# Kernel tuning notes

Hardware: AMD Instinct MI355X
Metric: run time of the kernel (lower is better)

The kernel has to match this reference:

```python
import jax, jax.numpy as jnp
import numpy as np

N_NODES = 100000
N_EDGES = 1250000
IN_DIM = 128
HID_DIM = 64
OUT_DIM = 16


def setup_inputs() -> dict:
    key = jax.random.key(0)
    k1, k2, k3, k4, k5, k6, k7 = jax.random.split(key, 7)
    x = jax.random.normal(k1, (N_NODES, IN_DIM), dtype=jnp.float32)
    edge_index = jax.random.randint(k2, (2, N_EDGES), 0, N_NODES, dtype=jnp.int64)
    s = 1.0 / np.sqrt(IN_DIM)
    W1 = jax.random.uniform(k3, (IN_DIM, HID_DIM), jnp.float32, -s, s)
    b1 = jax.random.uniform(k4, (HID_DIM,), jnp.float32, -s, s)
    s2 = 1.0 / np.sqrt(HID_DIM)
    W2 = jax.random.uniform(k5, (HID_DIM, OUT_DIM), jnp.float32, -s2, s2)
    b2 = jax.random.uniform(k6, (OUT_DIM,), jnp.float32, -s2, s2)
    return {"x": x, "edge_index": edge_index, "W1": W1, "b1": b1, "W2": W2, "b2": b2}


def reference(x, edge_index, W1, b1, W2, b2):
    # GCNConv (PyG default): linear transform, add self-loops, symmetric norm,
    # gather-scatter aggregation, bias. Then relu -> linear -> log_softmax.
    N = x.shape[0]
    loop = jnp.arange(N, dtype=edge_index.dtype)
    src = jnp.concatenate([edge_index[0], loop])  # message sources
    dst = jnpp_concat = jnp.concatenate([edge_index[1], loop])  # message targets
    # degree (with self-loops) computed on destination nodes
    deg = jax.ops.segment_sum(jnp.ones_like(dst, dtype=x.dtype), dst, num_segments=N)
    deg_inv_sqrt = jnp.where(deg > 0, jax.lax.rsqrt(deg), 0.0)
    norm = deg_inv_sqrt[src] * deg_inv_sqrt[dst]  # [E+N]
    h = x @ W1  # [N, hid] -- transform before aggregation (fewer bytes moved)
    msg = h[src] * norm[:, None]  # gather: [E+N, hid]
    agg = jax.ops.segment_sum(msg, dst, num_segments=N) + b1  # scatter-add
    h = jax.nn.relu(agg)
    logits = h @ W2 + b2
    return jax.nn.log_softmax(logits, axis=-1)
```

## Files before the change

kernel.cpp:

```cpp
#include <hip/hip_runtime.h>
#include <hip/hip_bf16.h>

#define N_NODES 100000
#define N_EDGES 1250000
#define IN_DIM  128
#define HID     64
#define OUTD    16
#define ROW     64
#define NRANGE  8
#define RSIZE   12500
#define NCHUNK  128
#define CHUNK   9768
#define FILLB   (NRANGE * NCHUNK)
#define MTILE   128
#define GEMMB   ((N_NODES + MTILE - 1) / MTILE)

typedef __attribute__((ext_vector_type(8))) short  short8;
typedef __attribute__((ext_vector_type(4))) float  floatx4;

__device__ __forceinline__ unsigned short f2bf(float f) {
    unsigned u = __float_as_uint(f);
    u += 0x7fffu + ((u >> 16) & 1u);
    return (unsigned short)(u >> 16);
}
__device__ __forceinline__ unsigned pk2(float lo, float hi) {
    __hip_bfloat162 t = __float22bfloat162_rn(make_float2(lo, hi));
    return *reinterpret_cast<unsigned*>(&t);
}
__device__ __forceinline__ float bf2f_lo(unsigned u) { return __uint_as_float(u << 16); }
__device__ __forceinline__ float bf2f_hi(unsigned u) { return __uint_as_float(u & 0xffff0000u); }

__global__ __launch_bounds__(256) void zero_cursor(int* __restrict__ cursor,
                                                   unsigned* __restrict__ hb_dummy) {
    int i = blockIdx.x * 256 + threadIdx.x;
    if (i < N_NODES) cursor[i] = 0;
    if (i < 32) hb_dummy[i] = 0u;
}

__global__ __launch_bounds__(256) void fill_gemm(const float* __restrict__ x,
                                                 const float* __restrict__ W1,
                                                 const int* __restrict__ src,
                                                 const int* __restrict__ dst,
                                                 int* __restrict__ cursor,
                                                 int* __restrict__ csr,
                                                 unsigned short* __restrict__ hb) {
    __shared__ unsigned short w1t[HID][132];

    if (blockIdx.x < FILLB) {
        const int r  = blockIdx.x & 7;
        const int c  = blockIdx.x >> 3;
        const int lo = r * RSIZE;
        const int q1 = min(N_EDGES, (c + 1) * CHUNK) >> 2;
        for (int q = (c * CHUNK >> 2) + threadIdx.x; q < q1; q += 256) {
            int4 d4 = ((const int4*)dst)[q];
            int  e  = q << 2;
#pragma unroll
            for (int u = 0; u < 4; u++) {
                int d = (u == 0) ? d4.x : (u == 1) ? d4.y : (u == 2) ? d4.z : d4.w;
                if ((unsigned)(d - lo) < (unsigned)RSIZE) {
                    int s = src[e + u];
                    int p = atomicAdd(&cursor[d], 1);
                    if (p < ROW) csr[(size_t)d * ROW + p] = s;
                }
            }
        }
        return;
    }

    const int m0 = (blockIdx.x - FILLB) * MTILE;

    for (int q = threadIdx.x; q < IN_DIM * HID / 4; q += 256) {
        int k = q >> 4, n = (q & 15) * 4;
        float4 wq = ((const float4*)W1)[q];
        w1t[n + 0][k] = f2bf(wq.x);
        w1t[n + 1][k] = f2bf(wq.y);
        w1t[n + 2][k] = f2bf(wq.z);
        w1t[n + 3][k] = f2bf(wq.w);
    }
    __syncthreads();

    const int lane = threadIdx.x & 63;
    const int w    = threadIdx.x >> 6;
    const int mrow = lane & 15;
    const int quad = lane >> 4;
    const int rowa = min(m0 + w * 32 + mrow,      N_NODES - 1);
    const int rowb = min(m0 + w * 32 + 16 + mrow, N_NODES - 1);

    floatx4 acc[2][4] = {};
#pragma unroll
    for (int k0 = 0; k0 < IN_DIM; k0 += 32) {
        union { unsigned u[4]; short8 s; } a0, a1;
        {
            const float4* pa = (const float4*)(x + (size_t)rowa * IN_DIM + k0 + quad * 8);
            float4 u0 = pa[0], v0 = pa[1];
            a0.u[0] = pk2(u0.x, u0.y); a0.u[1] = pk2(u0.z, u0.w);
            a0.u[2] = pk2(v0.x, v0.y); a0.u[3] = pk2(v0.z, v0.w);
            const float4* pb = (const float4*)(x + (size_t)rowb * IN_DIM + k0 + quad * 8);
            float4 u1 = pb[0], v1 = pb[1];
            a1.u[0] = pk2(u1.x, u1.y); a1.u[1] = pk2(u1.z, u1.w);
            a1.u[2] = pk2(v1.x, v1.y); a1.u[3] = pk2(v1.z, v1.w);
        }
        short8 b0 = *(const short8*)&w1t[ 0 + mrow][k0 + quad * 8];
        short8 b1 = *(const short8*)&w1t[16 + mrow][k0 + quad * 8];
        short8 b2 = *(const short8*)&w1t[32 + mrow][k0 + quad * 8];
        short8 b3 = *(const short8*)&w1t[48 + mrow][k0 + quad * 8];
        acc[0][0] = __builtin_amdgcn_mfma_f32_16x16x32_bf16(a0.s, b0, acc[0][0], 0, 0, 0);
        acc[0][1] = __builtin_amdgcn_mfma_f32_16x16x32_bf16(a0.s, b1, acc[0][1], 0, 0, 0);
        acc[0][2] = __builtin_amdgcn_mfma_f32_16x16x32_bf16(a0.s, b2, acc[0][2], 0, 0, 0);
        acc[0][3] = __builtin_amdgcn_mfma_f32_16x16x32_bf16(a0.s, b3, acc[0][3], 0, 0, 0);
        acc[1][0] = __builtin_amdgcn_mfma_f32_16x16x32_bf16(a1.s, b0, acc[1][0], 0, 0, 0);
        acc[1][1] = __builtin_amdgcn_mfma_f32_16x16x32_bf16(a1.s, b1, acc[1][1], 0, 0, 0);
        acc[1][2] = __builtin_amdgcn_mfma_f32_16x16x32_bf16(a1.s, b2, acc[1][2], 0, 0, 0);
        acc[1][3] = __builtin_amdgcn_mfma_f32_16x16x32_bf16(a1.s, b3, acc[1][3], 0, 0, 0);
    }

#pragma unroll
    for (int tm = 0; tm < 2; tm++) {
#pragma unroll
        for (int reg = 0; reg < 4; reg++) {
            int m = m0 + w * 32 + tm * 16 + quad * 4 + reg;
            if (m < N_NODES) {
#pragma unroll
                for (int tn = 0; tn < 4; tn++)
                    hb[(size_t)m * HID + tn * 16 + mrow] = f2bf(acc[tm][tn][reg]);
            }
        }
    }
}

__global__ __launch_bounds__(256) void pull_epilogue(const unsigned short* __restrict__ hb,
                                                     const int* __restrict__ csr,
                                                     const int* __restrict__ deg,
                                                     const float* __restrict__ b1,
                                                     const float* __restrict__ W2,
                                                     const float* __restrict__ b2,
                                                     float* __restrict__ out) {
    const int i     = blockIdx.x * 4 + (threadIdx.x >> 6);
    const int lane  = threadIdx.x & 63;
    const int e_sub = lane >> 4;
    const int f4    = lane & 15;

    const int   cnt = min(deg[i], ROW);
    const float di  = rsqrtf((float)deg[i] + 1.0f);

    int   s_l = N_NODES;
    float w_l = 0.f;
    if (lane < cnt) {
        s_l = csr[(size_t)i * ROW + lane];
        w_l = rsqrtf((float)deg[s_l] + 1.0f);
    }

    uint2 hs = ((const uint2*)(hb + (size_t)i * HID))[f4];

    float ax = 0.f, ay = 0.f, az = 0.f, aw = 0.f;
    const int G = (cnt + 3) >> 2;
    int g = 0;
    for (; g + 2 <= G; g += 2) {
        int e0 = (g << 2) + e_sub, e1 = e0 + 4;
        int   s0 = __shfl(s_l, e0, 64), s1 = __shfl(s_l, e1, 64);
        float w0 = __shfl(w_l, e0, 64), w1 = __shfl(w_l, e1, 64);
        uint2 a = ((const uint2*)(hb + (size_t)s0 * HID))[f4];
        uint2 b = ((const uint2*)(hb + (size_t)s1 * HID))[f4];
        ax = fmaf(bf2f_lo(a.x), w0, ax); ay = fmaf(bf2f_hi(a.x), w0, ay);
        az = fmaf(bf2f_lo(a.y), w0, az); aw = fmaf(bf2f_hi(a.y), w0, aw);
        ax = fmaf(bf2f_lo(b.x), w1, ax); ay = fmaf(bf2f_hi(b.x), w1, ay);
        az = fmaf(bf2f_lo(b.y), w1, az); aw = fmaf(bf2f_hi(b.y), w1, aw);
    }
    if (g < G) {
        int e0 = (g << 2) + e_sub;
        int   s0 = __shfl(s_l, e0, 64);
        float w0 = __shfl(w_l, e0, 64);
        uint2 a = ((const uint2*)(hb + (size_t)s0 * HID))[f4];
        ax = fmaf(bf2f_lo(a.x), w0, ax); ay = fmaf(bf2f_hi(a.x), w0, ay);
        az = fmaf(bf2f_lo(a.y), w0, az); aw = fmaf(bf2f_hi(a.y), w0, aw);
    }

    ax += __shfl_xor(ax, 16, 64); ax += __shfl_xor(ax, 32, 64);
    ay += __shfl_xor(ay, 16, 64); ay += __shfl_xor(ay, 32, 64);
    az += __shfl_xor(az, 16, 64); az += __shfl_xor(az, 32, 64);
    aw += __shfl_xor(aw, 16, 64); aw += __shfl_xor(aw, 32, 64);

    float4 b1v = ((const float4*)b1)[f4];
    float t0 = fmaf(bf2f_lo(hs.x), di, ax);
    float t1 = fmaf(bf2f_hi(hs.x), di, ay);
    float t2 = fmaf(bf2f_lo(hs.y), di, az);
    float t3 = fmaf(bf2f_hi(hs.y), di, aw);
    float v0 = fmaxf(fmaf(t0, di, b1v.x), 0.f);
    float v1 = fmaxf(fmaf(t1, di, b1v.y), 0.f);
    float v2 = fmaxf(fmaf(t2, di, b1v.z), 0.f);
    float v3 = fmaxf(fmaf(t3, di, b1v.w), 0.f);

    const float4* W2v = (const float4*)W2;
    float4 w0 = W2v[(4 * f4 + 0) * 4 + e_sub];
    float4 w1 = W2v[(4 * f4 + 1) * 4 + e_sub];
    float4 w2 = W2v[(4 * f4 + 2) * 4 + e_sub];
    float4 w3 = W2v[(4 * f4 + 3) * 4 + e_sub];
    float p0 = v0 * w0.x + v1 * w1.x + v2 * w2.x + v3 * w3.x;
    float p1 = v0 * w0.y + v1 * w1.y + v2 * w2.y + v3 * w3.y;
    float p2 = v0 * w0.z + v1 * w1.z + v2 * w2.z + v3 * w3.z;
    float p3 = v0 * w0.w + v1 * w1.w + v2 * w2.w + v3 * w3.w;
#pragma unroll
    for (int d = 1; d < 16; d <<= 1) {
        p0 += __shfl_xor(p0, d, 64);
        p1 += __shfl_xor(p1, d, 64);
        p2 += __shfl_xor(p2, d, 64);
        p3 += __shfl_xor(p3, d, 64);
    }
    float4 b2v = ((const float4*)b2)[e_sub];
    float lg0 = p0 + b2v.x, lg1 = p1 + b2v.y, lg2 = p2 + b2v.z, lg3 = p3 + b2v.w;

    float m = fmaxf(fmaxf(lg0, lg1), fmaxf(lg2, lg3));
    m = fmaxf(m, __shfl_xor(m, 16, 64));
    m = fmaxf(m, __shfl_xor(m, 32, 64));
    float s = __expf(lg0 - m) + __expf(lg1 - m) + __expf(lg2 - m) + __expf(lg3 - m);
    s += __shfl_xor(s, 16, 64);
    s += __shfl_xor(s, 32, 64);
    float lse = __logf(s) + m;

    if (f4 == 0) {
        float4 o = make_float4(lg0 - lse, lg1 - lse, lg2 - lse, lg3 - lse);
        ((float4*)out)[(size_t)i * 4 + e_sub] = o;
    }
}

extern "C" void kernel_launch(void* const* d_in, const int* in_sizes, int n_in,
                              void* d_out, int out_size, void* d_ws, size_t ws_size,
                              hipStream_t stream) {
    const float* x   = (const float*)d_in[0];
    const int*   ei  = (const int*)d_in[1];
    const float* W1  = (const float*)d_in[2];
    const float* b1  = (const float*)d_in[3];
    const float* W2  = (const float*)d_in[4];
    const float* b2  = (const float*)d_in[5];
    float*       out = (float*)d_out;

    const int* src = ei;
    const int* dst = ei + N_EDGES;

    char* ws = (char*)d_ws;
    size_t off = 0;
    unsigned short* hb = (unsigned short*)(ws + off);
    off += (size_t)(N_NODES + 1) * HID * 2;
    int*   csr    = (int*)  (ws + off); off += ((size_t)N_NODES * ROW + ROW) * 4;
    int*   cursor = (int*)  (ws + off); off += (size_t)N_NODES * 4;

    zero_cursor<<<(N_NODES + 255) / 256, 256, 0, stream>>>(
        cursor, (unsigned*)(hb + (size_t)N_NODES * HID));
    fill_gemm<<<FILLB + GEMMB, 256, 0, stream>>>(x, W1, src, dst, cursor, csr, hb);
    pull_epilogue<<<N_NODES / 4, 256, 0, stream>>>(hb, csr, cursor, b1, W2, b2, out);
}
```

Measured before the change: 231.2 us.

## Add nontemporal loads/stores, vectorize src reads, fold self-loop into gather loop

Edge src indices are now read as vectors alongside dst instead of per matching edge, and nontemporal hints are added to streaming loads and stores of x, edge lists, csr, hb writes and output. The pull kernel folds the self-loop into the neighbour list as an extra entry and unrolls the gather to four rows per iteration, with R rounded to 16-entry groups. This cuts scalar src loads and loop-tail overhead and aims to keep streamed data out of cache. In exchange, src is now read for every edge in all 8 range passes, and the per-node neighbour cap drops from 64 to 63.

```diff
diff --git a/kernel.cpp b/kernel.cpp
--- a/kernel.cpp
+++ b/kernel.cpp
@@ -17,6 +17,8 @@
 
 typedef __attribute__((ext_vector_type(8))) short  short8;
 typedef __attribute__((ext_vector_type(4))) float  floatx4;
+typedef __attribute__((ext_vector_type(4))) float  f32x4;
+typedef __attribute__((ext_vector_type(4))) int    i32x4;
 
 __device__ __forceinline__ unsigned short f2bf(float f) {
     unsigned u = __float_as_uint(f);
@@ -52,13 +54,13 @@
         const int lo = r * RSIZE;
         const int q1 = min(N_EDGES, (c + 1) * CHUNK) >> 2;
         for (int q = (c * CHUNK >> 2) + threadIdx.x; q < q1; q += 256) {
-            int4 d4 = ((const int4*)dst)[q];
-            int  e  = q << 2;
+            i32x4 d4 = __builtin_nontemporal_load(((const i32x4*)dst) + q);
+            i32x4 s4 = __builtin_nontemporal_load(((const i32x4*)src) + q);
 #pragma unroll
             for (int u = 0; u < 4; u++) {
                 int d = (u == 0) ? d4.x : (u == 1) ? d4.y : (u == 2) ? d4.z : d4.w;
+                int s = (u == 0) ? s4.x : (u == 1) ? s4.y : (u == 2) ? s4.z : s4.w;
                 if ((unsigned)(d - lo) < (unsigned)RSIZE) {
-                    int s = src[e + u];
                     int p = atomicAdd(&cursor[d], 1);
                     if (p < ROW) csr[(size_t)d * ROW + p] = s;
                 }
@@ -91,12 +93,14 @@
     for (int k0 = 0; k0 < IN_DIM; k0 += 32) {
         union { unsigned u[4]; short8 s; } a0, a1;
         {
-            const float4* pa = (const float4*)(x + (size_t)rowa * IN_DIM + k0 + quad * 8);
-            float4 u0 = pa[0], v0 = pa[1];
+            const f32x4* pa = (const f32x4*)(x + (size_t)rowa * IN_DIM + k0 + quad * 8);
+            f32x4 u0 = __builtin_nontemporal_load(pa);
+            f32x4 v0 = __builtin_nontemporal_load(pa + 1);
             a0.u[0] = pk2(u0.x, u0.y); a0.u[1] = pk2(u0.z, u0.w);
             a0.u[2] = pk2(v0.x, v0.y); a0.u[3] = pk2(v0.z, v0.w);
-            const float4* pb = (const float4*)(x + (size_t)rowb * IN_DIM + k0 + quad * 8);
-            float4 u1 = pb[0], v1 = pb[1];
+            const f32x4* pb = (const f32x4*)(x + (size_t)rowb * IN_DIM + k0 + quad * 8);
+            f32x4 u1 = __builtin_nontemporal_load(pb);
+            f32x4 v1 = __builtin_nontemporal_load(pb + 1);
             a1.u[0] = pk2(u1.x, u1.y); a1.u[1] = pk2(u1.z, u1.w);
             a1.u[2] = pk2(v1.x, v1.y); a1.u[3] = pk2(v1.z, v1.w);
         }
@@ -122,7 +126,8 @@
             if (m < N_NODES) {
 #pragma unroll
                 for (int tn = 0; tn < 4; tn++)
-                    hb[(size_t)m * HID + tn * 16 + mrow] = f2bf(acc[tm][tn][reg]);
+                    __builtin_nontemporal_store(f2bf(acc[tm][tn][reg]),
+                                                &hb[(size_t)m * HID + tn * 16 + mrow]);
             }
         }
     }
@@ -140,39 +145,42 @@
     const int e_sub = lane >> 4;
     const int f4    = lane & 15;
 
-    const int   cnt = min(deg[i], ROW);
-    const float di  = rsqrtf((float)deg[i] + 1.0f);
+    const int   dg  = deg[i];
+    const int   cnt = min(dg, ROW - 1);
+    const float di  = rsqrtf((float)dg + 1.0f);
 
     int   s_l = N_NODES;
     float w_l = 0.f;
     if (lane < cnt) {
-        s_l = csr[(size_t)i * ROW + lane];
+        s_l = __builtin_nontemporal_load(csr + (size_t)i * ROW + lane);
         w_l = rsqrtf((float)deg[s_l] + 1.0f);
-    }
-
-    uint2 hs = ((const uint2*)(hb + (size_t)i * HID))[f4];
+    } else if (lane == cnt) {
+        s_l = i;
+        w_l = di;
+    }
+
+    const uint2* hbv = (const uint2*)hb + f4;
 
     float ax = 0.f, ay = 0.f, az = 0.f, aw = 0.f;
-    const int G = (cnt + 3) >> 2;
-    int g = 0;
-    for (; g + 2 <= G; g += 2) {
-        int e0 = (g << 2) + e_sub, e1 = e0 + 4;
-        int   s0 = __shfl(s_l, e0, 64), s1 = __shfl(s_l, e1, 64);
-        float w0 = __shfl(w_l, e0, 64), w1 = __shfl(w_l, e1, 64);
-        uint2 a = ((const uint2*)(hb + (size_t)s0 * HID))[f4];
-        uint2 b = ((const uint2*)(hb + (size_t)s1 * HID))[f4];
+    const int R = (cnt + 16) >> 4;
+    for (int r = 0; r < R; ++r) {
+        const int e0 = (r << 4) + e_sub;
+        int   s0 = __shfl(s_l, e0,      64), s1 = __shfl(s_l, e0 + 4,  64);
+        int   s2 = __shfl(s_l, e0 + 8,  64), s3 = __shfl(s_l, e0 + 12, 64);
+        float w0 = __shfl(w_l, e0,      64), w1 = __shfl(w_l, e0 + 4,  64);
+        float w2 = __shfl(w_l, e0 + 8,  64), w3 = __shfl(w_l, e0 + 12, 64);
+        uint2 a = hbv[s0 << 4];
+        uint2 b = hbv[s1 << 4];
+        uint2 c = hbv[s2 << 4];
+        uint2 d = hbv[s3 << 4];
         ax = fmaf(bf2f_lo(a.x), w0, ax); ay = fmaf(bf2f_hi(a.x), w0, ay);
         az = fmaf(bf2f_lo(a.y), w0, az); aw = fmaf(bf2f_hi(a.y), w0, aw);
         ax = fmaf(bf2f_lo(b.x), w1, ax); ay = fmaf(bf2f_hi(b.x), w1, ay);
         az = fmaf(bf2f_lo(b.y), w1, az); aw = fmaf(bf2f_hi(b.y), w1, aw);
-    }
-    if (g < G) {
-        int e0 = (g << 2) + e_sub;
-        int   s0 = __shfl(s_l, e0, 64);
-        float w0 = __shfl(w_l, e0, 64);
-        uint2 a = ((const uint2*)(hb + (size_t)s0 * HID))[f4];
-        ax = fmaf(bf2f_lo(a.x), w0, ax); ay = fmaf(bf2f_hi(a.x), w0, ay);
-        az = fmaf(bf2f_lo(a.y), w0, az); aw = fmaf(bf2f_hi(a.y), w0, aw);
+        ax = fmaf(bf2f_lo(c.x), w2, ax); ay = fmaf(bf2f_hi(c.x), w2, ay);
+        az = fmaf(bf2f_lo(c.y), w2, az); aw = fmaf(bf2f_hi(c.y), w2, aw);
+        ax = fmaf(bf2f_lo(d.x), w3, ax); ay = fmaf(bf2f_hi(d.x), w3, ay);
+        az = fmaf(bf2f_lo(d.y), w3, az); aw = fmaf(bf2f_hi(d.y), w3, aw);
     }
 
     ax += __shfl_xor(ax, 16, 64); ax += __shfl_xor(ax, 32, 64);
@@ -181,14 +189,10 @@
     aw += __shfl_xor(aw, 16, 64); aw += __shfl_xor(aw, 32, 64);
 
     float4 b1v = ((const float4*)b1)[f4];
-    float t0 = fmaf(bf2f_lo(hs.x), di, ax);
-    float t1 = fmaf(bf2f_hi(hs.x), di, ay);
-    float t2 = fmaf(bf2f_lo(hs.y), di, az);
-    float t3 = fmaf(bf2f_hi(hs.y), di, aw);
-    float v0 = fmaxf(fmaf(t0, di, b1v.x), 0.f);
-    float v1 = fmaxf(fmaf(t1, di, b1v.y), 0.f);
-    float v2 = fmaxf(fmaf(t2, di, b1v.z), 0.f);
-    float v3 = fmaxf(fmaf(t3, di, b1v.w), 0.f);
+    float v0 = fmaxf(fmaf(ax, di, b1v.x), 0.f);
+    float v1 = fmaxf(fmaf(ay, di, b1v.y), 0.f);
+    float v2 = fmaxf(fmaf(az, di, b1v.z), 0.f);
+    float v3 = fmaxf(fmaf(aw, di, b1v.w), 0.f);
 
     const float4* W2v = (const float4*)W2;
     float4 w0 = W2v[(4 * f4 + 0) * 4 + e_sub];
@@ -218,8 +222,8 @@
     float lse = __logf(s) + m;
 
     if (f4 == 0) {
-        float4 o = make_float4(lg0 - lse, lg1 - lse, lg2 - lse, lg3 - lse);
-        ((float4*)out)[(size_t)i * 4 + e_sub] = o;
+        f32x4 o = {lg0 - lse, lg1 - lse, lg2 - lse, lg3 - lse};
+        __builtin_nontemporal_store(o, ((f32x4*)out) + (size_t)i * 4 + e_sub);
     }
 }
 
```

Measured after the change: 237.5 us. 1.03x slower.
